# Kernel tuning notes

Measured on AMD Instinct MI355X. Metric: run time of the kernel, lower is better.

The kernel has to match this reference:

```python
import jax, jax.numpy as jnp
import numpy as np

B, S, C, HD = 1, 2048, 2048, 128
H = C // HD  # 16 heads
EPS = float(jnp.finfo(jnp.float32).eps)  # torch nn.RMSNorm default eps


def setup_inputs() -> dict:
    key = jax.random.key(0)
    ks = jax.random.split(key, 10)
    std = 1.0 / np.sqrt(C)
    return {
        "x": jax.random.normal(ks[0], (B, S, C), jnp.float32),
        "rope": jax.random.normal(ks[1], (1, S, 1, HD // 2, 2, 2), jnp.float32),
        "wq": jax.random.normal(ks[2], (C, C), jnp.float32) * std,
        "bq": jax.random.normal(ks[3], (C,), jnp.float32) * 0.01,
        "wk": jax.random.normal(ks[4], (C, C), jnp.float32) * std,
        "bk": jax.random.normal(ks[5], (C,), jnp.float32) * 0.01,
        "wv": jax.random.normal(ks[6], (C, C), jnp.float32) * std,
        "bv": jax.random.normal(ks[7], (C,), jnp.float32) * 0.01,
        "q_norm_w": jnp.ones((HD,), jnp.float32),
        "k_norm_w": jnp.ones((HD,), jnp.float32),
        "wo": jax.random.normal(ks[8], (C, C), jnp.float32) * std,
        "bo": jax.random.normal(ks[9], (C,), jnp.float32) * 0.01,
    }


def _rmsnorm(x, w):
    # x: [..., HD]
    ms = jnp.mean(x * x, axis=-1, keepdims=True)
    return x * jax.lax.rsqrt(ms + EPS) * w


def _apply_rotary(x, rope):
    # x: [B,S,H,HD]; rope: [1,S,1,HD//2,2,2]
    shp = x.shape
    x_ = x.reshape(*shp[:-1], -1, 1, 2)          # [B,S,H,HD/2,1,2]
    out = (rope * x_).sum(axis=-1)               # [B,S,H,HD/2,2]
    return out.reshape(shp)


def reference(x, rope, wq, bq, wk, bk, wv, bv, q_norm_w, k_norm_w, wo, bo):
    q = x @ wq.T + bq
    k = x @ wk.T + bk
    v = x @ wv.T + bv
    q = q.reshape(B, S, H, HD)
    k = k.reshape(B, S, H, HD)
    v = v.reshape(B, S, H, HD)
    q = _rmsnorm(q, q_norm_w)
    k = _rmsnorm(k, k_norm_w)
    q = _apply_rotary(q, rope)
    k = _apply_rotary(k, rope)
    scale = 1.0 / np.sqrt(HD)
    scores = jnp.einsum("bqhd,bkhd->bhqk", q, k) * scale  # [B,H,S,S]
    attn = jax.nn.softmax(scores, axis=-1)
    out = jnp.einsum("bhqk,bkhd->bqhd", attn, v).reshape(B, S, C)
    return out @ wo.T + bo
```

## Files before the change

kernel.cpp:

```cpp
#include <hip/hip_runtime.h>
#include <stdint.h>

#define GLOBAL_AS __attribute__((address_space(1)))
#define LDS_AS    __attribute__((address_space(3)))

typedef unsigned short u16;
typedef __attribute__((ext_vector_type(8))) __bf16 bf16x8;
typedef __attribute__((ext_vector_type(4))) float   f32x4;
typedef __attribute__((ext_vector_type(2))) float   f32x2;
typedef __attribute__((ext_vector_type(4))) u16     u16x4;

#if __has_builtin(__builtin_amdgcn_exp2f)
#define EXP2(x) __builtin_amdgcn_exp2f(x)
#else
#define EXP2(x) __exp2f(x)
#endif

static __device__ __forceinline__ float bf2f(u16 u) {
    union { uint32_t i; float f; } c; c.i = ((uint32_t)u) << 16; return c.f;
}
static __device__ __forceinline__ u16 f2bf(float f) {
    union { float f; uint32_t i; } c; c.f = f;
    uint32_t r = c.i + 0x7fffu + ((c.i >> 16) & 1u);
    return (u16)(r >> 16);
}
static __device__ __forceinline__ u16 f2bf_fast(float f) {
    union { float f; uint32_t i; } c; c.f = f;
    return (u16)((c.i + 0x8000u) >> 16);
}
static __device__ __forceinline__ void gl_lds16(const void* g, void* l) {
    __builtin_amdgcn_global_load_lds((GLOBAL_AS const uint32_t*)g,
                                     (LDS_AS uint32_t*)l, 16, 0, 0);
}
static __device__ __forceinline__ f32x4 mfma16(bf16x8 a, bf16x8 b, f32x4 c) {
    return __builtin_amdgcn_mfma_f32_16x16x32_bf16(a, b, c, 0, 0, 0);
}

__global__ __launch_bounds__(256) void cast5(
    const float* __restrict__ s0, const float* __restrict__ s1,
    const float* __restrict__ s2, const float* __restrict__ s3,
    const float* __restrict__ s4,
    u16* __restrict__ d0, u16* __restrict__ d1, u16* __restrict__ d2,
    u16* __restrict__ d3, u16* __restrict__ d4)
{
    const float* s; u16* d;
    switch (blockIdx.y) {
        case 0: s = s0; d = d0; break;
        case 1: s = s1; d = d1; break;
        case 2: s = s2; d = d2; break;
        case 3: s = s3; d = d3; break;
        default: s = s4; d = d4; break;
    }
    int i = (blockIdx.x * 256 + threadIdx.x) * 4;
    f32x4 v = *(const f32x4*)&s[i];
    u16x4 u = { f2bf(v[0]), f2bf(v[1]), f2bf(v[2]), f2bf(v[3]) };
    *(u16x4*)&d[i] = u;
}

static __device__ __forceinline__ void stage_qkv(
    const u16* __restrict__ Ab,
    const u16* __restrict__ wq, const u16* __restrict__ wk, const u16* __restrict__ wv,
    int bn, int k0, u16* slot, int tid)
{
#pragma unroll
    for (int i = 0; i < 4; ++i) {
        int unit = i * 512 + tid;
        const u16* src;
        if (i < 2) {
            int row = unit >> 2, c = unit & 3;
            src = Ab + (size_t)row * 2048 + k0 + c * 8;
        } else {
            int ub = unit - 1024; if (ub > 767) ub = 767;
            int row = ub >> 2, c = ub & 3;
            int gr = bn * 192 + row;
            const u16* base = gr < 2048 ? wq : (gr < 4096 ? wk : wv);
            src = base + (size_t)(gr & 2047) * 2048 + k0 + c * 8;
        }
        gl_lds16(src, slot + unit * 8);
    }
}

__global__ __launch_bounds__(512, 2) void gemm_qkv3(
    const u16* __restrict__ x,
    const u16* __restrict__ wq, const u16* __restrict__ wk, const u16* __restrict__ wv,
    const float* __restrict__ bq, const float* __restrict__ bk, const float* __restrict__ bv,
    u16* __restrict__ q, u16* __restrict__ k, u16* __restrict__ v)
{
    __shared__ u16 SL[4][16384];
    const int tid = threadIdx.x, l = tid & 63, w = tid >> 6;
    const int wm = w >> 2, wn = w & 3;
    const int lr = l & 15, lg = l >> 4;
    const int bid = blockIdx.x;
    const int bm = bid & 7, bn = bid >> 3;

    const u16* Ab = x + (size_t)(bm * 256) * 2048;

    f32x4 acc[8][3];
#pragma unroll
    for (int mi = 0; mi < 8; ++mi)
#pragma unroll
        for (int nj = 0; nj < 3; ++nj) acc[mi][nj] = (f32x4){0.f, 0.f, 0.f, 0.f};

#pragma unroll
    for (int t = 0; t < 3; ++t)
        stage_qkv(Ab, wq, wk, wv, bn, t * 32, (u16*)SL[t], tid);

#pragma unroll 1
    for (int t = 0; t < 64; ++t) {
        const u16* As = (const u16*)SL[t & 3];
        const u16* Bs = As + 8192;
        const int tn = (t + 3 <= 63) ? (t + 3) : 63;

        asm volatile("s_waitcnt vmcnt(8)" ::: "memory");
        __builtin_amdgcn_s_barrier();
        __builtin_amdgcn_sched_barrier(0);

        stage_qkv(Ab, wq, wk, wv, bn, tn * 32, (u16*)SL[(t + 3) & 3], tid);

        bf16x8 a[8], b[3];
#pragma unroll
        for (int mi = 0; mi < 8; ++mi)
            a[mi] = *(const bf16x8*)&As[(wm * 128 + mi * 16 + lr) * 32 + lg * 8];
#pragma unroll
        for (int nj = 0; nj < 3; ++nj)
            b[nj] = *(const bf16x8*)&Bs[(wn * 48 + nj * 16 + lr) * 32 + lg * 8];
        __builtin_amdgcn_s_setprio(1);
#pragma unroll
        for (int mi = 0; mi < 8; ++mi)
#pragma unroll
            for (int nj = 0; nj < 3; ++nj)
                acc[mi][nj] = mfma16(a[mi], b[nj], acc[mi][nj]);
        __builtin_amdgcn_s_setprio(0);
    }
    asm volatile("s_waitcnt vmcnt(0)" ::: "memory");

#pragma unroll
    for (int mi = 0; mi < 8; ++mi) {
        int row0 = bm * 256 + wm * 128 + mi * 16 + lg * 4;
#pragma unroll
        for (int nj = 0; nj < 3; ++nj) {
            int col = bn * 192 + wn * 48 + nj * 16 + lr;
            int cs = (col >> 11), cc = col & 2047;
            u16* C = cs == 0 ? q : (cs == 1 ? k : v);
            const float* bp = cs == 0 ? bq : (cs == 1 ? bk : bv);
            float bs = bp[cc];
#pragma unroll
            for (int reg = 0; reg < 4; ++reg)
                C[(size_t)(row0 + reg) * 2048 + cc] = f2bf(acc[mi][nj][reg] + bs);
        }
    }
}

static __device__ __forceinline__ void stage_out(
    const u16* __restrict__ Ab, const u16* __restrict__ Bb,
    int k0, u16* slot, int tid)
{
    {
        int row = tid >> 2, c = tid & 3;
        gl_lds16(Ab + (size_t)row * 2048 + k0 + c * 8, slot + tid * 8);
    }
    {
        int row = tid >> 2, c = tid & 3;
        gl_lds16(Bb + (size_t)row * 2048 + k0 + c * 8, slot + 4096 + tid * 8);
    }
}

__global__ __launch_bounds__(512, 2) void gemm_out2(
    const u16* __restrict__ a, const u16* __restrict__ wo,
    const float* __restrict__ bo, float* __restrict__ out)
{
    __shared__ u16 SL[4][8192];
    const int tid = threadIdx.x, l = tid & 63, w = tid >> 6;
    const int wm = w >> 2, wn = w & 3;
    const int lr = l & 15, lg = l >> 4;
    const int bid = blockIdx.x;
    const int xcd = bid & 7, j = bid >> 3;
    const int bm = xcd * 2 + (j & 1), bn = j >> 1;

    const u16* Ab = a  + (size_t)(bm * 128) * 2048;
    const u16* Bb = wo + (size_t)(bn * 128) * 2048;

    f32x4 acc[4][2];
#pragma unroll
    for (int mi = 0; mi < 4; ++mi)
#pragma unroll
        for (int nj = 0; nj < 2; ++nj) acc[mi][nj] = (f32x4){0.f, 0.f, 0.f, 0.f};

#pragma unroll
    for (int t = 0; t < 3; ++t)
        stage_out(Ab, Bb, t * 32, (u16*)SL[t], tid);

#pragma unroll 1
    for (int t = 0; t < 64; ++t) {
        const u16* As = (const u16*)SL[t & 3];
        const u16* Bs = As + 4096;
        const int tn = (t + 3 <= 63) ? (t + 3) : 63;

        asm volatile("s_waitcnt vmcnt(4)" ::: "memory");
        __builtin_amdgcn_s_barrier();
        __builtin_amdgcn_sched_barrier(0);

        stage_out(Ab, Bb, tn * 32, (u16*)SL[(t + 3) & 3], tid);

        bf16x8 af[4], bf[2];
#pragma unroll
        for (int mi = 0; mi < 4; ++mi)
            af[mi] = *(const bf16x8*)&As[(wm * 64 + mi * 16 + lr) * 32 + lg * 8];
#pragma unroll
        for (int nj = 0; nj < 2; ++nj)
            bf[nj] = *(const bf16x8*)&Bs[(wn * 32 + nj * 16 + lr) * 32 + lg * 8];
        __builtin_amdgcn_s_setprio(1);
#pragma unroll
        for (int mi = 0; mi < 4; ++mi)
#pragma unroll
            for (int nj = 0; nj < 2; ++nj)
                acc[mi][nj] = mfma16(af[mi], bf[nj], acc[mi][nj]);
        __builtin_amdgcn_s_setprio(0);
    }
    asm volatile("s_waitcnt vmcnt(0)" ::: "memory");

#pragma unroll
    for (int mi = 0; mi < 4; ++mi) {
        int row0 = bm * 128 + wm * 64 + mi * 16 + lg * 4;
#pragma unroll
        for (int nj = 0; nj < 2; ++nj) {
            int col = bn * 128 + wn * 32 + nj * 16 + lr;
            float bs = bo[col];
#pragma unroll
            for (int reg = 0; reg < 4; ++reg)
                out[(size_t)(row0 + reg) * 2048 + col] = acc[mi][nj][reg] + bs;
        }
    }
}

__global__ __launch_bounds__(256) void norm_rope(
    const u16* __restrict__ qb, const u16* __restrict__ kb,
    const float* __restrict__ rope, const float* __restrict__ qw, const float* __restrict__ kw,
    u16* __restrict__ qh, u16* __restrict__ kh)
{
    const int tid = threadIdx.x, l = tid & 63, w = tid >> 6;
    const int rowid = blockIdx.x * 4 + w;
    const int h = rowid & 15, s = rowid >> 4;
    const size_t gbase = (size_t)s * 2048 + h * 128 + 2 * l;

    uint32_t qu = *(const uint32_t*)&qb[gbase];
    uint32_t ku = *(const uint32_t*)&kb[gbase];
    float q0 = bf2f((u16)qu), q1 = bf2f((u16)(qu >> 16));
    float k0 = bf2f((u16)ku), k1 = bf2f((u16)(ku >> 16));

    float sq = q0 * q0 + q1 * q1;
    float sk = k0 * k0 + k1 * k1;
#pragma unroll
    for (int m = 1; m < 64; m <<= 1) {
        sq += __shfl_xor(sq, m);
        sk += __shfl_xor(sk, m);
    }
    const float EPS = 1.1920928955078125e-07f;
    const float SCALE = 0.08838834764831845f * 1.4426950408889634f;
    float rq = rsqrtf(sq * (1.f / 128.f) + EPS) * SCALE;
    float rk = rsqrtf(sk * (1.f / 128.f) + EPS);

    f32x2 wq2 = *(const f32x2*)&qw[2 * l];
    f32x2 wk2 = *(const f32x2*)&kw[2 * l];
    float qn0 = q0 * rq * wq2[0], qn1 = q1 * rq * wq2[1];
    float kn0 = k0 * rk * wk2[0], kn1 = k1 * rk * wk2[1];

    f32x4 rr = *(const f32x4*)&rope[(size_t)s * 256 + l * 4];
    float qo0 = rr[0] * qn0 + rr[1] * qn1;
    float qo1 = rr[2] * qn0 + rr[3] * qn1;
    float ko0 = rr[0] * kn0 + rr[1] * kn1;
    float ko1 = rr[2] * kn0 + rr[3] * kn1;

    const size_t obase = ((size_t)h * 2048 + s) * 128 + 2 * l;
    *(uint32_t*)&qh[obase] = (uint32_t)f2bf(qo0) | ((uint32_t)f2bf(qo1) << 16);
    *(uint32_t*)&kh[obase] = (uint32_t)f2bf(ko0) | ((uint32_t)f2bf(ko1) << 16);
}

__global__ __launch_bounds__(256) void transpose_v(
    const u16* __restrict__ vb, u16* __restrict__ vt)
{
    __shared__ u16 t[64 * 80];
    const int h = blockIdx.z, s0 = blockIdx.x * 64, d0 = blockIdx.y * 64;
    const int tid = threadIdx.x;
#pragma unroll
    for (int cc = tid; cc < 512; cc += 256) {
        int r = cc >> 3, u = cc & 7;
        *(bf16x8*)&t[r * 80 + u * 8] =
            *(const bf16x8*)&vb[(size_t)(s0 + r) * 2048 + h * 128 + d0 + u * 8];
    }
    __syncthreads();
#pragma unroll
    for (int cc = tid; cc < 512; cc += 256) {
        int dr = cc >> 3, u = cc & 7;
        u16 vv[8];
#pragma unroll
        for (int j = 0; j < 8; ++j) vv[j] = t[(u * 8 + j) * 80 + dr];
        u16x4 lo = { vv[0], vv[1], vv[2], vv[3] };
        u16x4 hi = { vv[4], vv[5], vv[6], vv[7] };
        u16* dst = &vt[((size_t)h * 128 + d0 + dr) * 2048 + s0 + u * 8];
        *(u16x4*)dst = lo;
        *(u16x4*)(dst + 4) = hi;
    }
}

__global__ __launch_bounds__(256, 2) void attn(
    const u16* __restrict__ qh, const u16* __restrict__ kh,
    const u16* __restrict__ vt, float* __restrict__ Op, float* __restrict__ Lp)
{
    __shared__ u16 Ks[64 * 128];
    __shared__ u16 Vs[128 * 64];
    __shared__ u16 Ps[4][32 * 68];
    const int tid = threadIdx.x, l = tid & 63, w = tid >> 6;
    const int h = blockIdx.z, half = blockIdx.y;
    const int q0 = blockIdx.x * 128 + w * 32;
    const int lr = l & 15, lg = l >> 4;
    const float SHIFT = -17.312340490667562f;

    const u16* Kh = kh + (size_t)h * 2048 * 128;
    const u16* Vh = vt + (size_t)h * 128 * 2048;
    const int kvbase = half * 1024;

    bf16x8 qf[2][4];
#pragma unroll
    for (int am = 0; am < 2; ++am)
#pragma unroll
        for (int kk = 0; kk < 4; ++kk)
            qf[am][kk] = *(const bf16x8*)
                &qh[((size_t)h * 2048 + q0 + am * 16 + lr) * 128 + kk * 32 + lg * 8];

    bf16x8 onesf;
#pragma unroll
    for (int j = 0; j < 8; ++j) {
        union { u16 u; __bf16 b; } cb; cb.u = 0x3F80;
        onesf[j] = cb.b;
    }

    f32x4 o[2][8];
#pragma unroll
    for (int am = 0; am < 2; ++am)
#pragma unroll
        for (int dj = 0; dj < 8; ++dj) o[am][dj] = (f32x4){0.f, 0.f, 0.f, 0.f};
    f32x4 ol[2] = { (f32x4){0.f, 0.f, 0.f, 0.f}, (f32x4){0.f, 0.f, 0.f, 0.f} };

#pragma unroll 1
    for (int t = 0; t < 16; ++t) {
        const int kv0 = kvbase + t * 64;
        __syncthreads();
#pragma unroll
        for (int r = 0; r < 4; ++r) {
            int c = w * 4 + r;
            {
                int row = c * 4 + (l >> 4);
                int u = (l & 15) ^ (row & 7);
                gl_lds16(Kh + (size_t)(kv0 + row) * 128 + u * 8, &Ks[c * 512 + l * 8]);
            }
            {
                int row = c * 8 + (l >> 3);
                int u = (l & 7) ^ (row & 7);
                gl_lds16(Vh + (size_t)row * 2048 + kv0 + u * 8, &Vs[c * 512 + l * 8]);
            }
        }
        __syncthreads();

        f32x4 sc[2][4];
#pragma unroll
        for (int am = 0; am < 2; ++am)
#pragma unroll
            for (int nj = 0; nj < 4; ++nj)
                sc[am][nj] = (f32x4){SHIFT, SHIFT, SHIFT, SHIFT};
        __builtin_amdgcn_s_setprio(1);
#pragma unroll
        for (int kk = 0; kk < 4; ++kk)
#pragma unroll
            for (int nj = 0; nj < 4; ++nj) {
                int n = nj * 16 + lr;
                bf16x8 b = *(const bf16x8*)&Ks[n * 128 + ((kk * 4 + lg) ^ (n & 7)) * 8];
#pragma unroll
                for (int am = 0; am < 2; ++am)
                    sc[am][nj] = mfma16(qf[am][kk], b, sc[am][nj]);
            }
        __builtin_amdgcn_s_setprio(0);

#pragma unroll
        for (int am = 0; am < 2; ++am)
#pragma unroll
            for (int reg = 0; reg < 4; ++reg)
#pragma unroll
                for (int nj = 0; nj < 4; ++nj)
                    Ps[w][(am * 16 + lg * 4 + reg) * 68 + nj * 16 + lr] =
                        f2bf_fast(EXP2(sc[am][nj][reg]));
        asm volatile("s_waitcnt lgkmcnt(0)" ::: "memory");
        __builtin_amdgcn_sched_barrier(0);

        bf16x8 pa[2][2];
#pragma unroll
        for (int am = 0; am < 2; ++am)
#pragma unroll
            for (int kk2 = 0; kk2 < 2; ++kk2) {
                union { u16x4 h4[2]; bf16x8 v8; } cvt;
                cvt.h4[0] = *(const u16x4*)&Ps[w][(am * 16 + lr) * 68 + kk2 * 32 + lg * 8];
                cvt.h4[1] = *(const u16x4*)&Ps[w][(am * 16 + lr) * 68 + kk2 * 32 + lg * 8 + 4];
                pa[am][kk2] = cvt.v8;
            }
        __builtin_amdgcn_s_setprio(1);
#pragma unroll
        for (int am = 0; am < 2; ++am)
#pragma unroll
            for (int kk2 = 0; kk2 < 2; ++kk2)
                ol[am] = mfma16(pa[am][kk2], onesf, ol[am]);
#pragma unroll
        for (int dj = 0; dj < 8; ++dj)
#pragma unroll
            for (int kk2 = 0; kk2 < 2; ++kk2) {
                int n = dj * 16 + lr;
                bf16x8 b = *(const bf16x8*)&Vs[n * 64 + ((kk2 * 4 + lg) ^ (n & 7)) * 8];
#pragma unroll
                for (int am = 0; am < 2; ++am)
                    o[am][dj] = mfma16(pa[am][kk2], b, o[am][dj]);
            }
        __builtin_amdgcn_s_setprio(0);
    }

    if (lr == 0) {
#pragma unroll
        for (int am = 0; am < 2; ++am)
#pragma unroll
            for (int reg = 0; reg < 4; ++reg)
                Lp[(half * 16 + h) * 2048 + q0 + am * 16 + lg * 4 + reg] = ol[am][reg];
    }
#pragma unroll
    for (int am = 0; am < 2; ++am)
#pragma unroll
        for (int dj = 0; dj < 8; ++dj)
#pragma unroll
            for (int reg = 0; reg < 4; ++reg)
                Op[((size_t)half * 2048 + q0 + am * 16 + lg * 4 + reg) * 2048 +
                   h * 128 + dj * 16 + lr] = o[am][dj][reg];
}

__global__ __launch_bounds__(256) void combine(
    const float* __restrict__ Op, const float* __restrict__ Lp, u16* __restrict__ ab)
{
    int idx = (blockIdx.x * 256 + threadIdx.x) * 4;
    int s = idx >> 11, c = idx & 2047, h = c >> 7;
    f32x4 a = *(const f32x4*)&Op[(size_t)s * 2048 + c];
    f32x4 b = *(const f32x4*)&Op[(size_t)(2048 + s) * 2048 + c];
    float rl = 1.0f / (Lp[h * 2048 + s] + Lp[(16 + h) * 2048 + s]);
    u16x4 u = { f2bf((a[0] + b[0]) * rl), f2bf((a[1] + b[1]) * rl),
                f2bf((a[2] + b[2]) * rl), f2bf((a[3] + b[3]) * rl) };
    *(u16x4*)&ab[idx] = u;
}

extern "C" void kernel_launch(void* const* d_in, const int* in_sizes, int n_in,
                              void* d_out, int out_size, void* d_ws, size_t ws_size,
                              hipStream_t stream)
{
    (void)in_sizes; (void)n_in; (void)out_size;
    const float* x    = (const float*)d_in[0];
    const float* rope = (const float*)d_in[1];
    const float* wq   = (const float*)d_in[2];
    const float* bq   = (const float*)d_in[3];
    const float* wk   = (const float*)d_in[4];
    const float* bk   = (const float*)d_in[5];
    const float* wv   = (const float*)d_in[6];
    const float* bv   = (const float*)d_in[7];
    const float* qw   = (const float*)d_in[8];
    const float* kw   = (const float*)d_in[9];
    const float* wo   = (const float*)d_in[10];
    const float* bo   = (const float*)d_in[11];
    float* out = (float*)d_out;

    const size_t NE = 2048ull * 2048ull;
    if (ws_size < 13 * NE * 2) return;
    u16* p = (u16*)d_ws;
    u16* xb  = p; p += NE;
    u16* wqb = p; p += NE;
    u16* wkb = p; p += NE;
    u16* wvb = p; p += NE;
    u16* wob = p; p += NE;
    u16* qb  = p; p += NE;
    u16* kb  = p; p += NE;
    u16* vb  = p; p += NE;
    u16* qhb = p; p += NE;
    u16* khb = p; p += NE;
    u16* vhb = p; p += NE;
    u16* vtb = p; p += NE;
    u16* ab  = p; p += NE;
    (void)vhb;

    float* Op = (float*)xb;
    float* Lp = (float*)qb;

    cast5<<<dim3(4096, 5), 256, 0, stream>>>(x, wq, wk, wv, wo, xb, wqb, wkb, wvb, wob);
    gemm_qkv3<<<256, 512, 0, stream>>>(xb, wqb, wkb, wvb, bq, bk, bv, qb, kb, vb);
    norm_rope<<<8192, 256, 0, stream>>>(qb, kb, rope, qw, kw, qhb, khb);
    transpose_v<<<dim3(32, 2, 16), 256, 0, stream>>>(vb, vtb);
    attn<<<dim3(16, 2, 16), 256, 0, stream>>>(qhb, khb, vtb, Op, Lp);
    combine<<<4096, 256, 0, stream>>>(Op, Lp, ab);
    gemm_out2<<<256, 512, 0, stream>>>(ab, wob, bo, out);
}
```

Baseline: 170.3 us.

## Split GEMM inner loop into two barrier-separated halves and shrink out-proj block to 4 waves

The QKV GEMM main loop now loads the B fragments and half of the A fragments, issues the first set of MFMAs, then hits an extra barrier before loading the second half of A. This lowers peak register use and staggers LDS reads against MFMAs. The output projection GEMM moves from 8 to 4 waves per block, each wave owning a 64x64 tile instead of 64x32, with staging spread over 4 loads per thread and the same two-phase split. The cost is an extra barrier every K step and fewer waves available to hide latency in the output GEMM.

Measured after the change: 171.9 us. No clear change (+1.0%).

```diff
diff --git a/kernel.cpp b/kernel.cpp
--- a/kernel.cpp
+++ b/kernel.cpp
@@ -117,19 +117,33 @@
 
         stage_qkv(Ab, wq, wk, wv, bn, tn * 32, (u16*)SL[(t + 3) & 3], tid);
 
-        bf16x8 a[8], b[3];
-#pragma unroll
-        for (int mi = 0; mi < 8; ++mi)
-            a[mi] = *(const bf16x8*)&As[(wm * 128 + mi * 16 + lr) * 32 + lg * 8];
+        bf16x8 b[3], a0[4];
 #pragma unroll
         for (int nj = 0; nj < 3; ++nj)
             b[nj] = *(const bf16x8*)&Bs[(wn * 48 + nj * 16 + lr) * 32 + lg * 8];
+#pragma unroll
+        for (int mi = 0; mi < 4; ++mi)
+            a0[mi] = *(const bf16x8*)&As[(wm * 128 + mi * 16 + lr) * 32 + lg * 8];
         __builtin_amdgcn_s_setprio(1);
 #pragma unroll
-        for (int mi = 0; mi < 8; ++mi)
+        for (int mi = 0; mi < 4; ++mi)
 #pragma unroll
             for (int nj = 0; nj < 3; ++nj)
-                acc[mi][nj] = mfma16(a[mi], b[nj], acc[mi][nj]);
+                acc[mi][nj] = mfma16(a0[mi], b[nj], acc[mi][nj]);
+        __builtin_amdgcn_s_setprio(0);
+        __builtin_amdgcn_s_barrier();
+        __builtin_amdgcn_sched_barrier(0);
+
+        bf16x8 a1[4];
+#pragma unroll
+        for (int mi = 0; mi < 4; ++mi)
+            a1[mi] = *(const bf16x8*)&As[(wm * 128 + (4 + mi) * 16 + lr) * 32 + lg * 8];
+        __builtin_amdgcn_s_setprio(1);
+#pragma unroll
+        for (int mi = 0; mi < 4; ++mi)
+#pragma unroll
+            for (int nj = 0; nj < 3; ++nj)
+                acc[4 + mi][nj] = mfma16(a1[mi], b[nj], acc[4 + mi][nj]);
         __builtin_amdgcn_s_setprio(0);
     }
     asm volatile("s_waitcnt vmcnt(0)" ::: "memory");
@@ -155,23 +169,23 @@
     const u16* __restrict__ Ab, const u16* __restrict__ Bb,
     int k0, u16* slot, int tid)
 {
-    {
-        int row = tid >> 2, c = tid & 3;
-        gl_lds16(Ab + (size_t)row * 2048 + k0 + c * 8, slot + tid * 8);
-    }
-    {
-        int row = tid >> 2, c = tid & 3;
-        gl_lds16(Bb + (size_t)row * 2048 + k0 + c * 8, slot + 4096 + tid * 8);
-    }
-}
-
-__global__ __launch_bounds__(512, 2) void gemm_out2(
+#pragma unroll
+    for (int i = 0; i < 4; ++i) {
+        int unit = i * 256 + tid;
+        int ub = unit & 511;
+        int row = ub >> 2, c = ub & 3;
+        const u16* src = (unit < 512 ? Ab : Bb) + (size_t)row * 2048 + k0 + c * 8;
+        gl_lds16(src, slot + unit * 8);
+    }
+}
+
+__global__ __launch_bounds__(256, 2) void gemm_out3(
     const u16* __restrict__ a, const u16* __restrict__ wo,
     const float* __restrict__ bo, float* __restrict__ out)
 {
     __shared__ u16 SL[4][8192];
     const int tid = threadIdx.x, l = tid & 63, w = tid >> 6;
-    const int wm = w >> 2, wn = w & 3;
+    const int wm = w >> 1, wn = w & 1;
     const int lr = l & 15, lg = l >> 4;
     const int bid = blockIdx.x;
     const int xcd = bid & 7, j = bid >> 3;
@@ -180,11 +194,11 @@
     const u16* Ab = a  + (size_t)(bm * 128) * 2048;
     const u16* Bb = wo + (size_t)(bn * 128) * 2048;
 
-    f32x4 acc[4][2];
+    f32x4 acc[4][4];
 #pragma unroll
     for (int mi = 0; mi < 4; ++mi)
 #pragma unroll
-        for (int nj = 0; nj < 2; ++nj) acc[mi][nj] = (f32x4){0.f, 0.f, 0.f, 0.f};
+        for (int nj = 0; nj < 4; ++nj) acc[mi][nj] = (f32x4){0.f, 0.f, 0.f, 0.f};
 
 #pragma unroll
     for (int t = 0; t < 3; ++t)
@@ -196,25 +210,39 @@
         const u16* Bs = As + 4096;
         const int tn = (t + 3 <= 63) ? (t + 3) : 63;
 
-        asm volatile("s_waitcnt vmcnt(4)" ::: "memory");
+        asm volatile("s_waitcnt vmcnt(8)" ::: "memory");
         __builtin_amdgcn_s_barrier();
         __builtin_amdgcn_sched_barrier(0);
 
         stage_out(Ab, Bb, tn * 32, (u16*)SL[(t + 3) & 3], tid);
 
-        bf16x8 af[4], bf[2];
-#pragma unroll
-        for (int mi = 0; mi < 4; ++mi)
-            af[mi] = *(const bf16x8*)&As[(wm * 64 + mi * 16 + lr) * 32 + lg * 8];
-#pragma unroll
-        for (int nj = 0; nj < 2; ++nj)
-            bf[nj] = *(const bf16x8*)&Bs[(wn * 32 + nj * 16 + lr) * 32 + lg * 8];
+        bf16x8 bf[4], af0[2];
+#pragma unroll
+        for (int nj = 0; nj < 4; ++nj)
+            bf[nj] = *(const bf16x8*)&Bs[(wn * 64 + nj * 16 + lr) * 32 + lg * 8];
+#pragma unroll
+        for (int mi = 0; mi < 2; ++mi)
+            af0[mi] = *(const bf16x8*)&As[(wm * 64 + mi * 16 + lr) * 32 + lg * 8];
         __builtin_amdgcn_s_setprio(1);
 #pragma unroll
-        for (int mi = 0; mi < 4; ++mi)
-#pragma unroll
-            for (int nj = 0; nj < 2; ++nj)
-                acc[mi][nj] = mfma16(af[mi], bf[nj], acc[mi][nj]);
+        for (int mi = 0; mi < 2; ++mi)
+#pragma unroll
+            for (int nj = 0; nj < 4; ++nj)
+                acc[mi][nj] = mfma16(af0[mi], bf[nj], acc[mi][nj]);
+        __builtin_amdgcn_s_setprio(0);
+        __builtin_amdgcn_s_barrier();
+        __builtin_amdgcn_sched_barrier(0);
+
+        bf16x8 af1[2];
+#pragma unroll
+        for (int mi = 0; mi < 2; ++mi)
+            af1[mi] = *(const bf16x8*)&As[(wm * 64 + (2 + mi) * 16 + lr) * 32 + lg * 8];
+        __builtin_amdgcn_s_setprio(1);
+#pragma unroll
+        for (int mi = 0; mi < 2; ++mi)
+#pragma unroll
+            for (int nj = 0; nj < 4; ++nj)
+                acc[2 + mi][nj] = mfma16(af1[mi], bf[nj], acc[2 + mi][nj]);
         __builtin_amdgcn_s_setprio(0);
     }
     asm volatile("s_waitcnt vmcnt(0)" ::: "memory");
@@ -223,8 +251,8 @@
     for (int mi = 0; mi < 4; ++mi) {
         int row0 = bm * 128 + wm * 64 + mi * 16 + lg * 4;
 #pragma unroll
-        for (int nj = 0; nj < 2; ++nj) {
-            int col = bn * 128 + wn * 32 + nj * 16 + lr;
+        for (int nj = 0; nj < 4; ++nj) {
+            int col = bn * 128 + wn * 64 + nj * 16 + lr;
             float bs = bo[col];
 #pragma unroll
             for (int reg = 0; reg < 4; ++reg)
@@ -497,5 +525,5 @@
     transpose_v<<<dim3(32, 2, 16), 256, 0, stream>>>(vb, vtb);
     attn<<<dim3(16, 2, 16), 256, 0, stream>>>(qhb, khb, vtb, Op, Lp);
     combine<<<4096, 256, 0, stream>>>(Op, Lp, ab);
-    gemm_out2<<<256, 512, 0, stream>>>(ab, wob, bo, out);
-}
+    gemm_out3<<<256, 256, 0, stream>>>(ab, wob, bo, out);
+}
```
